# Performance work log

Hardware: AMD Instinct MI355X
Metric: run time of the kernel (lower is better)

Reference implementation:

```python
import jax, jax.numpy as jnp
import numpy as np
from jax import lax

B, N, F_IN, DIM = 128, 200, 200, 32
E_PER = 6400
K1, K2 = 100, 50
OUT = 2
BN_EPS = 1e-5


def setup_inputs():
    key = jax.random.key(0)
    ks = jax.random.split(key, 16)
    x = jax.random.normal(ks[0], (B * N, F_IN), jnp.float32)
    src = jax.random.randint(ks[1], (B, E_PER), 0, N)
    dst = jax.random.randint(ks[2], (B, E_PER), 0, N)
    off = (jnp.arange(B) * N)[:, None]
    edge_index = jnp.stack([(src + off).reshape(-1), (dst + off).reshape(-1)]).astype(jnp.int32)
    batch = jnp.repeat(jnp.arange(B, dtype=jnp.int32), N)

    def lin(k, i, o):
        kw, kb = jax.random.split(k)
        return (jax.random.normal(kw, (i, o), jnp.float32) / np.float32(np.sqrt(i)),
                jax.random.normal(kb, (o,), jnp.float32) * 0.01)

    w1a, b1a = lin(ks[3], F_IN, DIM)
    w1b, b1b = lin(ks[4], DIM, DIM)
    w2a, b2a = lin(ks[5], DIM, DIM)
    w2b, b2b = lin(ks[6], DIM, DIM)
    pw1 = jax.random.normal(ks[7], (DIM,), jnp.float32)
    pw2 = jax.random.normal(ks[8], (DIM,), jnp.float32)
    fc1_w, fc1_b = lin(ks[9], 2 * DIM, 4 * DIM)
    fc2_w, fc2_b = lin(ks[10], 4 * DIM, 8 * DIM)
    fc3_w, fc3_b = lin(ks[11], 8 * DIM, OUT)
    return dict(x=x, edge_index=edge_index, batch=batch,
                w1a=w1a, b1a=b1a, w1b=w1b, b1b=b1b,
                w2a=w2a, b2a=b2a, w2b=w2b, b2b=b2b,
                pw1=pw1, pw2=pw2,
                fc1_w=fc1_w, fc1_b=fc1_b, fc2_w=fc2_w, fc2_b=fc2_b,
                fc3_w=fc3_w, fc3_b=fc3_b,
                bn1_g=jnp.ones((4 * DIM,)), bn1_b=jnp.zeros((4 * DIM,)),
                bn1_m=jnp.zeros((4 * DIM,)), bn1_v=jnp.ones((4 * DIM,)),
                bn2_g=jnp.ones((8 * DIM,)), bn2_b=jnp.zeros((8 * DIM,)),
                bn2_m=jnp.zeros((8 * DIM,)), bn2_v=jnp.ones((8 * DIM,)))


def gin_conv(x, src, dst, valid, wa, ba, wb, bb, n_nodes):
    # PyG GINConv: mlp((1+eps)*x + sum_{j->i} x_j), eps=0 (default)
    msg = x[src]
    if valid is not None:
        msg = msg * valid[:, None]
    aggr = jax.ops.segment_sum(msg, dst, num_segments=n_nodes)
    h = jax.nn.relu((x + aggr) @ wa + ba)
    return h @ wb + bb


def topk_pool(x, src, dst, valid, pw, nb, n_per, k):
    # PyG TopKPooling: score = tanh((x.w)/||w||); keep top-k per graph; x <- x[perm]*score[perm]
    score = jnp.tanh((x @ pw) / jnp.linalg.norm(pw))
    topv, topi = lax.top_k(score.reshape(nb, n_per), k)  # [nb,k], descending (matches PyG ordering)
    perm = (topi + (jnp.arange(nb) * n_per)[:, None]).reshape(-1)
    x_new = x[perm] * topv.reshape(-1, 1)
    new_id = jnp.full((nb * n_per,), -1, jnp.int32).at[perm].set(jnp.arange(nb * k, dtype=jnp.int32))
    s, d = new_id[src], new_id[dst]
    v = (s >= 0) & (d >= 0)
    if valid is not None:
        v = v & valid
    return x_new, jnp.maximum(s, 0), jnp.maximum(d, 0), v, topv


def bn_eval(h, g, b, m, v):
    return (h - m) * lax.rsqrt(v + BN_EPS) * g + b


def reference(x, edge_index, batch,
              w1a, b1a, w1b, b1b, w2a, b2a, w2b, b2b, pw1, pw2,
              fc1_w, fc1_b, fc2_w, fc2_b, fc3_w, fc3_b,
              bn1_g, bn1_b, bn1_m, bn1_v, bn2_g, bn2_b, bn2_m, bn2_v):
    src, dst = edge_index[0], edge_index[1]
    h = jax.nn.relu(gin_conv(x, src, dst, None, w1a, b1a, w1b, b1b, B * N))
    h, src, dst, valid, attn1 = topk_pool(h, src, dst, None, pw1, B, N, K1)
    hb = h.reshape(B, K1, DIM)
    x1 = jnp.concatenate([hb.max(axis=1), hb.mean(axis=1)], axis=1)  # gmp || gap
    h = jax.nn.relu(gin_conv(h, src, dst, valid.astype(h.dtype), w2a, b2a, w2b, b2b, B * K1))
    h, src, dst, valid, attn2 = topk_pool(h, src, dst, valid, pw2, B, K1, K2)
    hb = h.reshape(B, K2, DIM)
    x2 = jnp.concatenate([hb.max(axis=1), hb.mean(axis=1)], axis=1)
    z = x1 + x2
    z = bn_eval(jax.nn.relu(z @ fc1_w + fc1_b), bn1_g, bn1_b, bn1_m, bn1_v)  # dropout p=0.6 inactive (eval)
    z = bn_eval(jax.nn.relu(z @ fc2_w + fc2_b), bn2_g, bn2_b, bn2_m, bn2_v)
    xy = jax.nn.log_softmax(z @ fc3_w + fc3_b, axis=-1)
    return xy, jax.nn.sigmoid(attn1), jax.nn.sigmoid(attn2)
```

## Files before the change

### kernel.cpp

```cpp
#include <hip/hip_runtime.h>
#include <math.h>

#define NGRAPH 128
#define NNODE  200
#define FIN    200
#define DIM    32
#define EPER   6400
#define ETOT   819200
#define KP1    100
#define KP2    50

#define W1B_OFF  0
#define W2A_OFF  1024
#define W2B_OFF  2048
#define B1A_OFF  3072
#define B1B_OFF  3104
#define B2A_OFF  3136
#define B2B_OFF  3168
#define PW1_OFF  3200
#define PW2_OFF  3232
#define NRM1_OFF 3264
#define NRM2_OFF 3265
#define SW_SIZE  3280

__device__ __forceinline__ int swz(int row, int chunk) {
  return (row << 5) + (((chunk ^ ((row >> 2) & 7))) << 2);
}

__device__ __forceinline__ void lds_spin(volatile int* f, int target) {
  while (*f != target) __builtin_amdgcn_s_sleep(2);
}

template <int ROWS, bool RELU, bool BIAS, bool FUSE, bool SCORE>
__device__ __forceinline__ void mm2r(const float* __restrict__ A,
                                     const float* __restrict__ A2,
                                     const float* __restrict__ fb,
                                     const float* __restrict__ W,
                                     float* __restrict__ O,
                                     const float* __restrict__ bias,
                                     const float* __restrict__ pw,
                                     const float* __restrict__ nrmp,
                                     float* __restrict__ scoreOut, int tid) {
  if (tid < ROWS * 2) {
    const int rg = tid >> 2, cg = tid & 3;
    const int r0 = rg * 2, d0 = cg * 8;
    float acc[2][8];
#pragma unroll
    for (int r = 0; r < 2; ++r)
#pragma unroll
      for (int c = 0; c < 8; ++c) acc[r][c] = 0.f;
#pragma unroll
    for (int kc = 0; kc < 8; ++kc) {
      float4 av[2];
#pragma unroll
      for (int r = 0; r < 2; ++r) {
        const int p = swz(r0 + r, kc);
        float4 v = *(const float4*)&A[p];
        if (FUSE) {
          const float4 u = *(const float4*)&A2[p];
          const float4 b = *(const float4*)&fb[kc * 4];
          v.x = fmaxf(v.x + u.x + b.x, 0.f);
          v.y = fmaxf(v.y + u.y + b.y, 0.f);
          v.z = fmaxf(v.z + u.z + b.z, 0.f);
          v.w = fmaxf(v.w + u.w + b.w, 0.f);
        }
        av[r] = v;
      }
#pragma unroll
      for (int j = 0; j < 4; ++j) {
        const int k = kc * 4 + j;
        const float4 wa = *(const float4*)&W[k * 32 + d0];
        const float4 wb = *(const float4*)&W[k * 32 + d0 + 4];
#pragma unroll
        for (int r = 0; r < 2; ++r) {
          const float xs = (j == 0) ? av[r].x : (j == 1) ? av[r].y
                                  : (j == 2) ? av[r].z : av[r].w;
          acc[r][0] += xs * wa.x; acc[r][1] += xs * wa.y;
          acc[r][2] += xs * wa.z; acc[r][3] += xs * wa.w;
          acc[r][4] += xs * wb.x; acc[r][5] += xs * wb.y;
          acc[r][6] += xs * wb.z; acc[r][7] += xs * wb.w;
        }
      }
    }
    float dot[2] = {0.f, 0.f};
#pragma unroll
    for (int r = 0; r < 2; ++r) {
      float v[8];
#pragma unroll
      for (int c = 0; c < 8; ++c) {
        float t = acc[r][c];
        if (BIAS) t += bias[d0 + c];
        if (RELU) t = fmaxf(t, 0.f);
        v[c] = t;
      }
      if (SCORE) {
        float d = 0.f;
#pragma unroll
        for (int c = 0; c < 8; ++c) d += v[c] * pw[d0 + c];
        dot[r] = d;
      }
      float4 o0, o1;
      o0.x = v[0]; o0.y = v[1]; o0.z = v[2]; o0.w = v[3];
      o1.x = v[4]; o1.y = v[5]; o1.z = v[6]; o1.w = v[7];
      *(float4*)&O[swz(r0 + r, cg * 2)] = o0;
      *(float4*)&O[swz(r0 + r, cg * 2 + 1)] = o1;
    }
    if (SCORE) {
      dot[0] += __shfl_xor(dot[0], 1); dot[0] += __shfl_xor(dot[0], 2);
      dot[1] += __shfl_xor(dot[1], 1); dot[1] += __shfl_xor(dot[1], 2);
      if ((tid & 3) == 0) {
        const float nrm = *nrmp;
        scoreOut[r0] = tanhf(dot[0] / nrm);
        scoreOut[r0 + 1] = tanhf(dot[1] / nrm);
      }
    }
  }
}

__device__ __forceinline__ void scan_counts(const int* __restrict__ cnt,
                                            int* __restrict__ start, int lane) {
  const int b = lane * 4;
  const int c0 = (cnt[b + 0] + 3) & ~3;
  const int c1 = (cnt[b + 1] + 3) & ~3;
  const int c2 = (cnt[b + 2] + 3) & ~3;
  const int c3 = (cnt[b + 3] + 3) & ~3;
  const int t01 = c0 + c1;
  const int t012 = t01 + c2;
  const int tot = t012 + c3;
  int run = tot;
#pragma unroll
  for (int off = 1; off < 64; off <<= 1) {
    const int t = __shfl_up(run, off);
    if (lane >= off) run += t;
  }
  const int e = run - tot;
  start[b + 0] = e;
  start[b + 1] = e + c0;
  start[b + 2] = e + t01;
  start[b + 3] = e + t012;
}

template <int NN>
__device__ __forceinline__ void aggregate(const float* __restrict__ sYv,
                                          float* __restrict__ sAgv,
                                          const int* __restrict__ sSrcv,
                                          const int* __restrict__ sStartv,
                                          const int* __restrict__ sCntv, int tid) {
  const int slot = tid >> 3, part = tid & 7;
#pragma unroll
  for (int p = 0; p < (NN + 127) / 128; ++p) {
    const int n = p * 128 + slot;
    if (n < NN) {
      const int jb = sStartv[n];
      const int je = jb + sCntv[n];
      float4 a0 = {0, 0, 0, 0}, a1 = {0, 0, 0, 0}, a2 = {0, 0, 0, 0}, a3 = {0, 0, 0, 0};
      int j = jb;
      for (; j + 4 <= je; j += 4) {
        const int4 ss = *(const int4*)&sSrcv[j];
        const float4 v0 = *(const float4*)&sYv[swz(ss.x, part)];
        const float4 v1 = *(const float4*)&sYv[swz(ss.y, part)];
        const float4 v2 = *(const float4*)&sYv[swz(ss.z, part)];
        const float4 v3 = *(const float4*)&sYv[swz(ss.w, part)];
        a0.x += v0.x; a0.y += v0.y; a0.z += v0.z; a0.w += v0.w;
        a1.x += v1.x; a1.y += v1.y; a1.z += v1.z; a1.w += v1.w;
        a2.x += v2.x; a2.y += v2.y; a2.z += v2.z; a2.w += v2.w;
        a3.x += v3.x; a3.y += v3.y; a3.z += v3.z; a3.w += v3.w;
      }
      for (; j < je; ++j) {
        const float4 v = *(const float4*)&sYv[swz(sSrcv[j], part)];
        a0.x += v.x; a0.y += v.y; a0.z += v.z; a0.w += v.w;
      }
      float4 o;
      o.x = (a0.x + a1.x) + (a2.x + a3.x);
      o.y = (a0.y + a1.y) + (a2.y + a3.y);
      o.z = (a0.z + a1.z) + (a2.z + a3.z);
      o.w = (a0.w + a1.w) + (a2.w + a3.w);
      *(float4*)&sAgv[swz(n, part)] = o;
    }
  }
}

__global__ __launch_bounds__(1024, 1) void gin_fused(
    const float* __restrict__ x, const int* __restrict__ ei,
    const float* __restrict__ w1a, const float* __restrict__ b1a,
    const float* __restrict__ w1b, const float* __restrict__ b1b,
    const float* __restrict__ w2a, const float* __restrict__ b2a,
    const float* __restrict__ w2b, const float* __restrict__ b2b,
    const float* __restrict__ pw1, const float* __restrict__ pw2,
    const float* __restrict__ fc1w, const float* __restrict__ fc1b,
    const float* __restrict__ fc2w, const float* __restrict__ fc2b,
    const float* __restrict__ fc3w, const float* __restrict__ fc3b,
    const float* __restrict__ bn1g, const float* __restrict__ bn1b,
    const float* __restrict__ bn1m, const float* __restrict__ bn1v,
    const float* __restrict__ bn2g, const float* __restrict__ bn2b,
    const float* __restrict__ bn2m, const float* __restrict__ bn2v,
    float* __restrict__ out) {
  __shared__ __align__(16) float sY[6400];
  __shared__ __align__(16) float sAg[6400];
  __shared__ __align__(16) float sH[6400];
  __shared__ __align__(16) float sHp[3200];
  __shared__ __align__(16) float sW[SW_SIZE];
  __shared__ __align__(16) int sSrc[7040];
  __shared__ unsigned short sEdge[6400];
  __shared__ int sCnt[256], sStart[256], sOfs[256];
  __shared__ int sCnt2[256], sStart2[256], sOfs2[256];
  __shared__ int sFlag[4];
  __shared__ float sScore[256];
  __shared__ int sNewid[256];
  __shared__ float sZ[64];
  __shared__ float sZ1[128];
  __shared__ float sZ2[256];
  __shared__ float sLg[2];

  const int tid = threadIdx.x;
  const int g = blockIdx.x;

  if (tid < 256) {
    for (int i = tid; i < 1600; i += 256)
      *(float4*)&sAg[i * 4] = ((const float4*)w1a)[i];
    if (tid < 32) {
      sW[B1A_OFF + tid] = b1a[tid];
      sW[B1B_OFF + tid] = b1b[tid];
      sW[B2A_OFF + tid] = b2a[tid];
      sW[B2B_OFF + tid] = b2b[tid];
      sW[PW1_OFF + tid] = pw1[tid];
      sW[PW2_OFF + tid] = pw2[tid];
    }
  } else if (tid < 512) {
    const int t = tid - 256;
    for (int i = t; i < 768; i += 256) {
      const float4 v = (i < 256) ? ((const float4*)w1b)[i]
                    : (i < 512) ? ((const float4*)w2a)[i - 256]
                                : ((const float4*)w2b)[i - 512];
      const int off = (i < 256) ? W1B_OFF + i * 4
                    : (i < 512) ? W2A_OFF + (i - 256) * 4
                                : W2B_OFF + (i - 512) * 4;
      *(float4*)&sW[off] = v;
    }
    for (int i = t; i < 256; i += 256) {
      sCnt[i] = 0; sOfs[i] = 0; sCnt2[i] = 0; sOfs2[i] = 0;
    }
    if (t < 4) sFlag[t] = 0;
  } else {
    const int eb = g * EPER, nb = g * NNODE;
    for (int i = tid - 512; i < EPER / 4; i += 512) {
      const int4 ss = *(const int4*)&ei[eb + i * 4];
      const int4 dd = *(const int4*)&ei[ETOT + eb + i * 4];
      sEdge[i * 4 + 0] = (unsigned short)(((ss.x - nb) << 8) | (dd.x - nb));
      sEdge[i * 4 + 1] = (unsigned short)(((ss.y - nb) << 8) | (dd.y - nb));
      sEdge[i * 4 + 2] = (unsigned short)(((ss.z - nb) << 8) | (dd.z - nb));
      sEdge[i * 4 + 3] = (unsigned short)(((ss.w - nb) << 8) | (dd.w - nb));
    }
  }
  __syncthreads();

  if (tid < 200) {
    const int rg = tid >> 2, cg = tid & 3;
    const int n0 = rg * 4, d0 = cg * 8;
    float acc[4][8];
#pragma unroll
    for (int r = 0; r < 4; ++r)
#pragma unroll
      for (int c = 0; c < 8; ++c) acc[r][c] = 0.f;
    const float* xg = x + ((size_t)g * NNODE + n0) * FIN;
    for (int k = 0; k < FIN; k += 4) {
      float4 xv[4];
#pragma unroll
      for (int r = 0; r < 4; ++r)
        xv[r] = *(const float4*)&xg[r * FIN + k];
#pragma unroll
      for (int j = 0; j < 4; ++j) {
        const float4 wa = *(const float4*)&sAg[(k + j) * 32 + d0];
        const float4 wb = *(const float4*)&sAg[(k + j) * 32 + d0 + 4];
#pragma unroll
        for (int r = 0; r < 4; ++r) {
          const float xs = (j == 0) ? xv[r].x : (j == 1) ? xv[r].y
                                   : (j == 2) ? xv[r].z : xv[r].w;
          acc[r][0] += xs * wa.x; acc[r][1] += xs * wa.y;
          acc[r][2] += xs * wa.z; acc[r][3] += xs * wa.w;
          acc[r][4] += xs * wb.x; acc[r][5] += xs * wb.y;
          acc[r][6] += xs * wb.z; acc[r][7] += xs * wb.w;
        }
      }
    }
#pragma unroll
    for (int r = 0; r < 4; ++r) {
      float4 o0, o1;
      o0.x = acc[r][0]; o0.y = acc[r][1]; o0.z = acc[r][2]; o0.w = acc[r][3];
      o1.x = acc[r][4]; o1.y = acc[r][5]; o1.z = acc[r][6]; o1.w = acc[r][7];
      *(float4*)&sY[swz(n0 + r, cg * 2)] = o0;
      *(float4*)&sY[swz(n0 + r, cg * 2 + 1)] = o1;
    }
  } else if (tid == 200) {
    float s = 0.f;
    for (int k = 0; k < 32; ++k) s += sW[PW1_OFF + k] * sW[PW1_OFF + k];
    sW[NRM1_OFF] = sqrtf(s);
  } else if (tid == 201) {
    float s = 0.f;
    for (int k = 0; k < 32; ++k) s += sW[PW2_OFF + k] * sW[PW2_OFF + k];
    sW[NRM2_OFF] = sqrtf(s);
  } else if (tid >= 256) {
    const int t = tid - 256;
    for (int e = t; e < EPER; e += 768)
      atomicAdd(&sCnt[sEdge[e] & 255], 1);
    __threadfence_block();
    atomicAdd(&sFlag[0], 1);
    if (tid >= 960) {
      lds_spin(&sFlag[0], 768);
      __threadfence_block();
      scan_counts(sCnt, sStart, tid - 960);
      __threadfence_block();
      if (tid == 960) atomicExch(&sFlag[1], 1);
    }
    lds_spin(&sFlag[1], 1);
    __threadfence_block();
    for (int e = t; e < EPER; e += 768) {
      const unsigned short p = sEdge[e];
      sSrc[sStart[p & 255] + atomicAdd(&sOfs[p & 255], 1)] = p >> 8;
    }
  }
  __syncthreads();

  aggregate<NNODE>(sY, sAg, sSrc, sStart, sCnt, tid);
  __syncthreads();

  mm2r<200, true, true, true, true>(sY, sAg, &sW[B1A_OFF], &sW[W1B_OFF], sH,
                                    &sW[B1B_OFF], &sW[PW1_OFF], &sW[NRM1_OFF],
                                    sScore, tid);
  __syncthreads();

  if (tid < NNODE * 4) {
    const int n = tid >> 2, q = tid & 3;
    const float s = sScore[n];
    int r = 0;
    for (int m = q * 50; m < q * 50 + 50; ++m) {
      const float sm = sScore[m];
      r += (sm > s) || (sm == s && m < n);
    }
    r += __shfl_xor(r, 1);
    r += __shfl_xor(r, 2);
    if (q == 0) {
      sNewid[n] = (r < KP1) ? r : -1;
      if (r < KP1) out[2 * NGRAPH + g * KP1 + r] = 1.f / (1.f + expf(-s));
    }
    if (r < KP1) {
#pragma unroll
      for (int c = 0; c < 2; ++c) {
        const int ch = q * 2 + c;
        float4 v = *(const float4*)&sH[swz(n, ch)];
        v.x *= s; v.y *= s; v.z *= s; v.w *= s;
        *(float4*)&sHp[swz(r, ch)] = v;
      }
    }
  }
  __syncthreads();

  mm2r<KP1, false, false, false, false>(sHp, nullptr, nullptr, &sW[W2A_OFF],
                                        sY, nullptr, nullptr, nullptr, nullptr,
                                        tid);
  if (tid >= 256 && tid < 288) {
    const int t = tid - 256;
    const int ch = t >> 2, w = t & 3;
    float m0 = -INFINITY, m1 = -INFINITY, s0 = 0.f, s1 = 0.f;
    for (int r = 0; r < KP1; r += 2) {
      const float v0 = sHp[swz(r, ch) + w];
      const float v1 = sHp[swz(r + 1, ch) + w];
      m0 = fmaxf(m0, v0); m1 = fmaxf(m1, v1);
      s0 += v0; s1 += v1;
    }
    sZ[t] = fmaxf(m0, m1);
    sZ[32 + t] = (s0 + s1) / (float)KP1;
  } else if (tid >= 512) {
    const int t = tid - 512;
    for (int e = t; e < EPER; e += 512) {
      const unsigned short p = sEdge[e];
      const int s1 = sNewid[p >> 8], d1 = sNewid[p & 255];
      if (s1 >= 0 && d1 >= 0) atomicAdd(&sCnt2[d1], 1);
    }
    __threadfence_block();
    atomicAdd(&sFlag[2], 1);
    if (tid >= 960) {
      lds_spin(&sFlag[2], 512);
      __threadfence_block();
      scan_counts(sCnt2, sStart2, tid - 960);
      __threadfence_block();
      if (tid == 960) atomicExch(&sFlag[3], 1);
    }
    lds_spin(&sFlag[3], 1);
    __threadfence_block();
    for (int e = t; e < EPER; e += 512) {
      const unsigned short p = sEdge[e];
      const int s1 = sNewid[p >> 8], d1 = sNewid[p & 255];
      if (s1 >= 0 && d1 >= 0)
        sSrc[sStart2[d1] + atomicAdd(&sOfs2[d1], 1)] = s1;
    }
  }
  __syncthreads();

  aggregate<KP1>(sY, sAg, sSrc, sStart2, sCnt2, tid);
  __syncthreads();

  mm2r<KP1, true, true, true, true>(sY, sAg, &sW[B2A_OFF], &sW[W2B_OFF], sH,
                                    &sW[B2B_OFF], &sW[PW2_OFF], &sW[NRM2_OFF],
                                    sScore, tid);
  __syncthreads();

  if (tid < KP1 * 4) {
    const int n = tid >> 2, q = tid & 3;
    const float s = sScore[n];
    int r = 0;
    for (int m = q * 25; m < q * 25 + 25; ++m) {
      const float sm = sScore[m];
      r += (sm > s) || (sm == s && m < n);
    }
    r += __shfl_xor(r, 1);
    r += __shfl_xor(r, 2);
    if (q == 0) {
      sNewid[n] = (r < KP2) ? r : -1;
      if (r < KP2)
        out[2 * NGRAPH + NGRAPH * KP1 + g * KP2 + r] = 1.f / (1.f + expf(-s));
    }
    if (r < KP2) {
#pragma unroll
      for (int c = 0; c < 2; ++c) {
        const int ch = q * 2 + c;
        float4 v = *(const float4*)&sH[swz(n, ch)];
        v.x *= s; v.y *= s; v.z *= s; v.w *= s;
        *(float4*)&sHp[swz(r, ch)] = v;
      }
    }
  }
  __syncthreads();

  if (tid < 32) {
    const int ch = tid >> 2, w = tid & 3;
    float m0 = -INFINITY, m1 = -INFINITY, s0 = 0.f, s1 = 0.f;
    for (int r = 0; r < KP2; r += 2) {
      const float v0 = sHp[swz(r, ch) + w];
      const float v1 = sHp[swz(r + 1, ch) + w];
      m0 = fmaxf(m0, v0); m1 = fmaxf(m1, v1);
      s0 += v0; s1 += v1;
    }
    sZ[tid] += fmaxf(m0, m1);
    sZ[32 + tid] += (s0 + s1) / (float)KP2;
  }
  __syncthreads();

  if (tid < 512) {
    const int o = tid >> 2, q = tid & 3;
    float a = 0.f;
    for (int k = q * 16; k < q * 16 + 16; ++k) a += sZ[k] * fc1w[k * 128 + o];
    a += __shfl_xor(a, 1);
    a += __shfl_xor(a, 2);
    if (q == 0) {
      a += fc1b[o];
      a = fmaxf(a, 0.f);
      a = (a - bn1m[o]) * rsqrtf(bn1v[o] + 1e-5f) * bn1g[o] + bn1b[o];
      sZ1[o] = a;
    }
  }
  __syncthreads();

  if (tid < 512) {
    const int o = tid >> 1, h = tid & 1;
    float a = 0.f;
    for (int k = h * 64; k < h * 64 + 64; ++k) a += sZ1[k] * fc2w[k * 256 + o];
    a += __shfl_xor(a, 1);
    if (h == 0) {
      a += fc2b[o];
      a = fmaxf(a, 0.f);
      a = (a - bn2m[o]) * rsqrtf(bn2v[o] + 1e-5f) * bn2g[o] + bn2b[o];
      sZ2[o] = a;
    }
  }
  __syncthreads();

  if (tid < 64) {
    const int k4 = tid * 4;
    float a0 = 0.f, a1 = 0.f;
#pragma unroll
    for (int k = 0; k < 4; ++k) {
      const float z = sZ2[k4 + k];
      a0 += z * fc3w[(k4 + k) * 2 + 0];
      a1 += z * fc3w[(k4 + k) * 2 + 1];
    }
#pragma unroll
    for (int off = 32; off; off >>= 1) {
      a0 += __shfl_xor(a0, off);
      a1 += __shfl_xor(a1, off);
    }
    if (tid == 0) {
      const float l0 = a0 + fc3b[0], l1 = a1 + fc3b[1];
      const float m = fmaxf(l0, l1);
      const float lse = m + logf(expf(l0 - m) + expf(l1 - m));
      out[g * 2 + 0] = l0 - lse;
      out[g * 2 + 1] = l1 - lse;
    }
  }
}

extern "C" void kernel_launch(void* const* d_in, const int* in_sizes, int n_in,
                              void* d_out, int out_size, void* d_ws,
                              size_t ws_size, hipStream_t stream) {
  (void)in_sizes; (void)n_in; (void)out_size; (void)d_ws; (void)ws_size;
  gin_fused<<<NGRAPH, 1024, 0, stream>>>(
      (const float*)d_in[0], (const int*)d_in[1],
      (const float*)d_in[3], (const float*)d_in[4],
      (const float*)d_in[5], (const float*)d_in[6],
      (const float*)d_in[7], (const float*)d_in[8],
      (const float*)d_in[9], (const float*)d_in[10],
      (const float*)d_in[11], (const float*)d_in[12],
      (const float*)d_in[13], (const float*)d_in[14],
      (const float*)d_in[15], (const float*)d_in[16],
      (const float*)d_in[17], (const float*)d_in[18],
      (const float*)d_in[19], (const float*)d_in[20],
      (const float*)d_in[21], (const float*)d_in[22],
      (const float*)d_in[23], (const float*)d_in[24],
      (const float*)d_in[25], (const float*)d_in[26],
      (float*)d_out);
}
```

Before: 52.75 us.

## Split first-layer projection into producer blocks with global flag handoff

Launches twice as many blocks. The first 128 blocks compute the x@w1a projection for each graph using all 800 threads and write it to workspace, then release a per-graph flag. The consumer blocks build the CSR in parallel, spin on the flag, and load the projection from global memory. The LDS spin-flag coordination is replaced with plain barriers, and the pooling reductions are split across two segments. This spreads the large input GEMM across more CUs, at the cost of an extra memset, a global round trip, and a deadlock risk if consumer blocks get scheduled before their producers.

```diff
diff --git a/kernel.cpp b/kernel.cpp
--- a/kernel.cpp
+++ b/kernel.cpp
@@ -25,10 +25,6 @@
 
 __device__ __forceinline__ int swz(int row, int chunk) {
   return (row << 5) + (((chunk ^ ((row >> 2) & 7))) << 2);
-}
-
-__device__ __forceinline__ void lds_spin(volatile int* f, int target) {
-  while (*f != target) __builtin_amdgcn_s_sleep(2);
 }
 
 template <int ROWS, bool RELU, bool BIAS, bool FUSE, bool SCORE>
@@ -194,6 +190,7 @@
     const float* __restrict__ bn1m, const float* __restrict__ bn1v,
     const float* __restrict__ bn2g, const float* __restrict__ bn2b,
     const float* __restrict__ bn2m, const float* __restrict__ bn2v,
+    int* __restrict__ flags, float* __restrict__ y1ws,
     float* __restrict__ out) {
   __shared__ __align__(16) float sY[6400];
   __shared__ __align__(16) float sAg[6400];
@@ -204,28 +201,60 @@
   __shared__ unsigned short sEdge[6400];
   __shared__ int sCnt[256], sStart[256], sOfs[256];
   __shared__ int sCnt2[256], sStart2[256], sOfs2[256];
-  __shared__ int sFlag[4];
   __shared__ float sScore[256];
   __shared__ int sNewid[256];
   __shared__ float sZ[64];
   __shared__ float sZ1[128];
   __shared__ float sZ2[256];
-  __shared__ float sLg[2];
 
   const int tid = threadIdx.x;
-  const int g = blockIdx.x;
+  const int bid = blockIdx.x;
+
+  if (bid < NGRAPH) {
+    const int g = bid;
+    for (int i = tid; i < 1600; i += 1024)
+      ((float4*)sAg)[i] = ((const float4*)w1a)[i];
+    __syncthreads();
+    if (tid < 800) {
+      const int rg = tid >> 3, cg = tid & 7;
+      const int n0 = rg * 2, d0 = cg * 4;
+      float a0[4] = {0, 0, 0, 0}, a1[4] = {0, 0, 0, 0};
+      const float* xg = x + ((size_t)g * NNODE + n0) * FIN;
+      for (int k = 0; k < FIN; k += 4) {
+        const float4 xa = *(const float4*)&xg[k];
+        const float4 xb = *(const float4*)&xg[FIN + k];
+#pragma unroll
+        for (int j = 0; j < 4; ++j) {
+          const float4 w = *(const float4*)&sAg[(k + j) * 32 + d0];
+          const float s0 = (j == 0) ? xa.x : (j == 1) ? xa.y
+                         : (j == 2) ? xa.z : xa.w;
+          const float s1 = (j == 0) ? xb.x : (j == 1) ? xb.y
+                         : (j == 2) ? xb.z : xb.w;
+          a0[0] += s0 * w.x; a0[1] += s0 * w.y;
+          a0[2] += s0 * w.z; a0[3] += s0 * w.w;
+          a1[0] += s1 * w.x; a1[1] += s1 * w.y;
+          a1[2] += s1 * w.z; a1[3] += s1 * w.w;
+        }
+      }
+      float* yg = y1ws + (size_t)g * 6400;
+      float4 o;
+      o.x = a0[0]; o.y = a0[1]; o.z = a0[2]; o.w = a0[3];
+      *(float4*)&yg[swz(n0, cg)] = o;
+      o.x = a1[0]; o.y = a1[1]; o.z = a1[2]; o.w = a1[3];
+      *(float4*)&yg[swz(n0 + 1, cg)] = o;
+    }
+    __threadfence();
+    __syncthreads();
+    if (tid == 0)
+      __hip_atomic_store(&flags[g], 1, __ATOMIC_RELEASE,
+                         __HIP_MEMORY_SCOPE_AGENT);
+    return;
+  }
+
+  const int g = bid - NGRAPH;
 
   if (tid < 256) {
-    for (int i = tid; i < 1600; i += 256)
-      *(float4*)&sAg[i * 4] = ((const float4*)w1a)[i];
-    if (tid < 32) {
-      sW[B1A_OFF + tid] = b1a[tid];
-      sW[B1B_OFF + tid] = b1b[tid];
-      sW[B2A_OFF + tid] = b2a[tid];
-      sW[B2B_OFF + tid] = b2b[tid];
-      sW[PW1_OFF + tid] = pw1[tid];
-      sW[PW2_OFF + tid] = pw2[tid];
-    }
+    sCnt[tid] = 0; sOfs[tid] = 0; sCnt2[tid] = 0; sOfs2[tid] = 0;
   } else if (tid < 512) {
     const int t = tid - 256;
     for (int i = t; i < 768; i += 256) {
@@ -237,10 +266,14 @@
                                 : W2B_OFF + (i - 512) * 4;
       *(float4*)&sW[off] = v;
     }
-    for (int i = t; i < 256; i += 256) {
-      sCnt[i] = 0; sOfs[i] = 0; sCnt2[i] = 0; sOfs2[i] = 0;
-    }
-    if (t < 4) sFlag[t] = 0;
+    if (t < 32) {
+      sW[B1A_OFF + t] = b1a[t];
+      sW[B1B_OFF + t] = b1b[t];
+      sW[B2A_OFF + t] = b2a[t];
+      sW[B2B_OFF + t] = b2b[t];
+      sW[PW1_OFF + t] = pw1[t];
+      sW[PW2_OFF + t] = pw2[t];
+    }
   } else {
     const int eb = g * EPER, nb = g * NNODE;
     for (int i = tid - 512; i < EPER / 4; i += 512) {
@@ -254,70 +287,45 @@
   }
   __syncthreads();
 
-  if (tid < 200) {
-    const int rg = tid >> 2, cg = tid & 3;
-    const int n0 = rg * 4, d0 = cg * 8;
-    float acc[4][8];
-#pragma unroll
-    for (int r = 0; r < 4; ++r)
-#pragma unroll
-      for (int c = 0; c < 8; ++c) acc[r][c] = 0.f;
-    const float* xg = x + ((size_t)g * NNODE + n0) * FIN;
-    for (int k = 0; k < FIN; k += 4) {
-      float4 xv[4];
-#pragma unroll
-      for (int r = 0; r < 4; ++r)
-        xv[r] = *(const float4*)&xg[r * FIN + k];
-#pragma unroll
-      for (int j = 0; j < 4; ++j) {
-        const float4 wa = *(const float4*)&sAg[(k + j) * 32 + d0];
-        const float4 wb = *(const float4*)&sAg[(k + j) * 32 + d0 + 4];
-#pragma unroll
-        for (int r = 0; r < 4; ++r) {
-          const float xs = (j == 0) ? xv[r].x : (j == 1) ? xv[r].y
-                                   : (j == 2) ? xv[r].z : xv[r].w;
-          acc[r][0] += xs * wa.x; acc[r][1] += xs * wa.y;
-          acc[r][2] += xs * wa.z; acc[r][3] += xs * wa.w;
-          acc[r][4] += xs * wb.x; acc[r][5] += xs * wb.y;
-          acc[r][6] += xs * wb.z; acc[r][7] += xs * wb.w;
-        }
-      }
-    }
-#pragma unroll
-    for (int r = 0; r < 4; ++r) {
-      float4 o0, o1;
-      o0.x = acc[r][0]; o0.y = acc[r][1]; o0.z = acc[r][2]; o0.w = acc[r][3];
-      o1.x = acc[r][4]; o1.y = acc[r][5]; o1.z = acc[r][6]; o1.w = acc[r][7];
-      *(float4*)&sY[swz(n0 + r, cg * 2)] = o0;
-      *(float4*)&sY[swz(n0 + r, cg * 2 + 1)] = o1;
-    }
-  } else if (tid == 200) {
+  if (tid < 800) {
+    const uint4 u = *(const uint4*)&sEdge[tid * 8];
+    atomicAdd(&sCnt[u.x & 255], 1);
+    atomicAdd(&sCnt[(u.x >> 16) & 255], 1);
+    atomicAdd(&sCnt[u.y & 255], 1);
+    atomicAdd(&sCnt[(u.y >> 16) & 255], 1);
+    atomicAdd(&sCnt[u.z & 255], 1);
+    atomicAdd(&sCnt[(u.z >> 16) & 255], 1);
+    atomicAdd(&sCnt[u.w & 255], 1);
+    atomicAdd(&sCnt[(u.w >> 16) & 255], 1);
+  } else if (tid == 1022) {
     float s = 0.f;
     for (int k = 0; k < 32; ++k) s += sW[PW1_OFF + k] * sW[PW1_OFF + k];
     sW[NRM1_OFF] = sqrtf(s);
-  } else if (tid == 201) {
+  } else if (tid == 1023) {
     float s = 0.f;
     for (int k = 0; k < 32; ++k) s += sW[PW2_OFF + k] * sW[PW2_OFF + k];
     sW[NRM2_OFF] = sqrtf(s);
-  } else if (tid >= 256) {
-    const int t = tid - 256;
-    for (int e = t; e < EPER; e += 768)
-      atomicAdd(&sCnt[sEdge[e] & 255], 1);
-    __threadfence_block();
-    atomicAdd(&sFlag[0], 1);
-    if (tid >= 960) {
-      lds_spin(&sFlag[0], 768);
-      __threadfence_block();
-      scan_counts(sCnt, sStart, tid - 960);
-      __threadfence_block();
-      if (tid == 960) atomicExch(&sFlag[1], 1);
-    }
-    lds_spin(&sFlag[1], 1);
-    __threadfence_block();
-    for (int e = t; e < EPER; e += 768) {
+  }
+  __syncthreads();
+
+  if (tid < 64) scan_counts(sCnt, sStart, tid);
+  __syncthreads();
+
+  if (tid < 1020) {
+    for (int e = tid; e < EPER; e += 1020) {
       const unsigned short p = sEdge[e];
       sSrc[sStart[p & 255] + atomicAdd(&sOfs[p & 255], 1)] = p >> 8;
     }
+  } else if (tid == 1023) {
+    while (__hip_atomic_load(&flags[g], __ATOMIC_ACQUIRE,
+                             __HIP_MEMORY_SCOPE_AGENT) == 0)
+      __builtin_amdgcn_s_sleep(8);
+  }
+  __syncthreads();
+
+  {
+    const float4* src = (const float4*)(y1ws + (size_t)g * 6400);
+    for (int i = tid; i < 1600; i += 1024) ((float4*)sY)[i] = src[i];
   }
   __syncthreads();
 
@@ -358,42 +366,38 @@
   mm2r<KP1, false, false, false, false>(sHp, nullptr, nullptr, &sW[W2A_OFF],
                                         sY, nullptr, nullptr, nullptr, nullptr,
                                         tid);
-  if (tid >= 256 && tid < 288) {
-    const int t = tid - 256;
-    const int ch = t >> 2, w = t & 3;
-    float m0 = -INFINITY, m1 = -INFINITY, s0 = 0.f, s1 = 0.f;
-    for (int r = 0; r < KP1; r += 2) {
-      const float v0 = sHp[swz(r, ch) + w];
-      const float v1 = sHp[swz(r + 1, ch) + w];
-      m0 = fmaxf(m0, v0); m1 = fmaxf(m1, v1);
-      s0 += v0; s1 += v1;
-    }
-    sZ[t] = fmaxf(m0, m1);
-    sZ[32 + t] = (s0 + s1) / (float)KP1;
+  if (tid >= 256 && tid < 320) {
+    const int l = tid - 256;
+    const int idx = l & 31, seg = l >> 5;
+    const int ch = idx >> 2, w = idx & 3;
+    float m = -INFINITY, s = 0.f;
+    for (int r = seg * 50; r < seg * 50 + 50; ++r) {
+      const float v = sHp[swz(r, ch) + w];
+      m = fmaxf(m, v); s += v;
+    }
+    m = fmaxf(m, __shfl_xor(m, 32));
+    s += __shfl_xor(s, 32);
+    if (seg == 0) {
+      sZ[idx] = m;
+      sZ[32 + idx] = s / (float)KP1;
+    }
   } else if (tid >= 512) {
-    const int t = tid - 512;
-    for (int e = t; e < EPER; e += 512) {
+    for (int e = tid - 512; e < EPER; e += 512) {
       const unsigned short p = sEdge[e];
       const int s1 = sNewid[p >> 8], d1 = sNewid[p & 255];
       if (s1 >= 0 && d1 >= 0) atomicAdd(&sCnt2[d1], 1);
     }
-    __threadfence_block();
-    atomicAdd(&sFlag[2], 1);
-    if (tid >= 960) {
-      lds_spin(&sFlag[2], 512);
-      __threadfence_block();
-      scan_counts(sCnt2, sStart2, tid - 960);
-      __threadfence_block();
-      if (tid == 960) atomicExch(&sFlag[3], 1);
-    }
-    lds_spin(&sFlag[3], 1);
-    __threadfence_block();
-    for (int e = t; e < EPER; e += 512) {
-      const unsigned short p = sEdge[e];
-      const int s1 = sNewid[p >> 8], d1 = sNewid[p & 255];
-      if (s1 >= 0 && d1 >= 0)
-        sSrc[sStart2[d1] + atomicAdd(&sOfs2[d1], 1)] = s1;
-    }
+  }
+  __syncthreads();
+
+  if (tid < 64) scan_counts(sCnt2, sStart2, tid);
+  __syncthreads();
+
+  for (int e = tid; e < EPER; e += 1024) {
+    const unsigned short p = sEdge[e];
+    const int s1 = sNewid[p >> 8], d1 = sNewid[p & 255];
+    if (s1 >= 0 && d1 >= 0)
+      sSrc[sStart2[d1] + atomicAdd(&sOfs2[d1], 1)] = s1;
   }
   __syncthreads();
 
@@ -432,17 +436,20 @@
   }
   __syncthreads();
 
-  if (tid < 32) {
-    const int ch = tid >> 2, w = tid & 3;
-    float m0 = -INFINITY, m1 = -INFINITY, s0 = 0.f, s1 = 0.f;
-    for (int r = 0; r < KP2; r += 2) {
-      const float v0 = sHp[swz(r, ch) + w];
-      const float v1 = sHp[swz(r + 1, ch) + w];
-      m0 = fmaxf(m0, v0); m1 = fmaxf(m1, v1);
-      s0 += v0; s1 += v1;
-    }
-    sZ[tid] += fmaxf(m0, m1);
-    sZ[32 + tid] += (s0 + s1) / (float)KP2;
+  if (tid < 64) {
+    const int idx = tid & 31, seg = tid >> 5;
+    const int ch = idx >> 2, w = idx & 3;
+    float m = -INFINITY, s = 0.f;
+    for (int r = seg * 25; r < seg * 25 + 25; ++r) {
+      const float v = sHp[swz(r, ch) + w];
+      m = fmaxf(m, v); s += v;
+    }
+    m = fmaxf(m, __shfl_xor(m, 32));
+    s += __shfl_xor(s, 32);
+    if (seg == 0) {
+      sZ[idx] += m;
+      sZ[32 + idx] += s / (float)KP2;
+    }
   }
   __syncthreads();
 
@@ -502,8 +509,11 @@
 extern "C" void kernel_launch(void* const* d_in, const int* in_sizes, int n_in,
                               void* d_out, int out_size, void* d_ws,
                               size_t ws_size, hipStream_t stream) {
-  (void)in_sizes; (void)n_in; (void)out_size; (void)d_ws; (void)ws_size;
-  gin_fused<<<NGRAPH, 1024, 0, stream>>>(
+  (void)in_sizes; (void)n_in; (void)out_size; (void)ws_size;
+  int* flags = (int*)d_ws;
+  float* y1ws = (float*)((char*)d_ws + 4096);
+  hipMemsetAsync(d_ws, 0, 4096, stream);
+  gin_fused<<<2 * NGRAPH, 1024, 0, stream>>>(
       (const float*)d_in[0], (const int*)d_in[1],
       (const float*)d_in[3], (const float*)d_in[4],
       (const float*)d_in[5], (const float*)d_in[6],
@@ -517,5 +527,5 @@
       (const float*)d_in[21], (const float*)d_in[22],
       (const float*)d_in[23], (const float*)d_in[24],
       (const float*)d_in[25], (const float*)d_in[26],
-      (float*)d_out);
+      flags, y1ws, (float*)d_out);
 }
```

Result: slower. 139.5 us (+164.4%).

## Replace block barriers with wave-level flags and fuse MLP head into one wave

Applied to the files above, without the earlier changes.

The first layer's prologue now uses per-wave LDS flag counters instead of a full __syncthreads. The w1a load gates the node GEMM directly, and the edge-load, histogram, scan and CSR-fill stages run on the other waves concurrently, with the remaining weight loads deferred to after the CSR fill. The GEMM K-loop is unrolled by 8, and pooling reductions are split across two half-waves with a shuffle combine. The fc1/fc2/fc3 head is collapsed into a single 64-thread wave so three block barriers disappear. This removes barrier stalls and tail latency but serialises the head MLP onto fewer threads with longer loops.

```diff
diff --git a/kernel.cpp b/kernel.cpp
--- a/kernel.cpp
+++ b/kernel.cpp
@@ -27,8 +27,10 @@
   return (row << 5) + (((chunk ^ ((row >> 2) & 7))) << 2);
 }
 
-__device__ __forceinline__ void lds_spin(volatile int* f, int target) {
-  while (*f != target) __builtin_amdgcn_s_sleep(2);
+__device__ __forceinline__ void spin_eq(const int* f, int target) {
+  while (__hip_atomic_load(f, __ATOMIC_RELAXED,
+                           __HIP_MEMORY_SCOPE_WORKGROUP) != target)
+    __builtin_amdgcn_s_sleep(1);
 }
 
 template <int ROWS, bool RELU, bool BIAS, bool FUSE, bool SCORE>
@@ -204,119 +206,140 @@
   __shared__ unsigned short sEdge[6400];
   __shared__ int sCnt[256], sStart[256], sOfs[256];
   __shared__ int sCnt2[256], sStart2[256], sOfs2[256];
-  __shared__ int sFlag[4];
+  __shared__ int sFlag[8];
   __shared__ float sScore[256];
   __shared__ int sNewid[256];
   __shared__ float sZ[64];
   __shared__ float sZ1[128];
-  __shared__ float sZ2[256];
-  __shared__ float sLg[2];
 
   const int tid = threadIdx.x;
+  const int lane = tid & 63;
   const int g = blockIdx.x;
+
+  if (tid < 8) sFlag[tid] = 0;
+  __syncthreads();
 
   if (tid < 256) {
     for (int i = tid; i < 1600; i += 256)
-      *(float4*)&sAg[i * 4] = ((const float4*)w1a)[i];
-    if (tid < 32) {
-      sW[B1A_OFF + tid] = b1a[tid];
-      sW[B1B_OFF + tid] = b1b[tid];
-      sW[B2A_OFF + tid] = b2a[tid];
-      sW[B2B_OFF + tid] = b2b[tid];
-      sW[PW1_OFF + tid] = pw1[tid];
-      sW[PW2_OFF + tid] = pw2[tid];
-    }
-  } else if (tid < 512) {
+      ((float4*)sAg)[i] = ((const float4*)w1a)[i];
+    __threadfence_block();
+    if (lane == 0) atomicAdd(&sFlag[0], 1);
+    spin_eq(&sFlag[0], 4);
+    if (tid < 200) {
+      const int rg = tid >> 2, cg = tid & 3;
+      const int n0 = rg * 4, d0 = cg * 8;
+      float acc[4][8];
+#pragma unroll
+      for (int r = 0; r < 4; ++r)
+#pragma unroll
+        for (int c = 0; c < 8; ++c) acc[r][c] = 0.f;
+      const float* xg = x + ((size_t)g * NNODE + n0) * FIN;
+      for (int k = 0; k < FIN; k += 8) {
+        float4 xv[4][2];
+#pragma unroll
+        for (int r = 0; r < 4; ++r) {
+          xv[r][0] = *(const float4*)&xg[r * FIN + k];
+          xv[r][1] = *(const float4*)&xg[r * FIN + k + 4];
+        }
+#pragma unroll
+        for (int h = 0; h < 2; ++h) {
+#pragma unroll
+          for (int j = 0; j < 4; ++j) {
+            const int kk = k + h * 4 + j;
+            const float4 wa = *(const float4*)&sAg[kk * 32 + d0];
+            const float4 wb = *(const float4*)&sAg[kk * 32 + d0 + 4];
+#pragma unroll
+            for (int r = 0; r < 4; ++r) {
+              const float xs = (j == 0) ? xv[r][h].x : (j == 1) ? xv[r][h].y
+                             : (j == 2) ? xv[r][h].z : xv[r][h].w;
+              acc[r][0] += xs * wa.x; acc[r][1] += xs * wa.y;
+              acc[r][2] += xs * wa.z; acc[r][3] += xs * wa.w;
+              acc[r][4] += xs * wb.x; acc[r][5] += xs * wb.y;
+              acc[r][6] += xs * wb.z; acc[r][7] += xs * wb.w;
+            }
+          }
+        }
+      }
+#pragma unroll
+      for (int r = 0; r < 4; ++r) {
+        float4 o0, o1;
+        o0.x = acc[r][0]; o0.y = acc[r][1]; o0.z = acc[r][2]; o0.w = acc[r][3];
+        o1.x = acc[r][4]; o1.y = acc[r][5]; o1.z = acc[r][6]; o1.w = acc[r][7];
+        *(float4*)&sY[swz(n0 + r, cg * 2)] = o0;
+        *(float4*)&sY[swz(n0 + r, cg * 2 + 1)] = o1;
+      }
+    } else {
+      const int t = tid - 200;
+      if (t < 32) {
+        sW[B1A_OFF + t] = b1a[t];
+        sW[B1B_OFF + t] = b1b[t];
+        sW[B2A_OFF + t] = b2a[t];
+        sW[B2B_OFF + t] = b2b[t];
+        sW[PW1_OFF + t] = pw1[t];
+        sW[PW2_OFF + t] = pw2[t];
+      }
+      __threadfence_block();
+      if (tid == 232) {
+        float s = 0.f;
+        for (int k = 0; k < 32; ++k) s += sW[PW1_OFF + k] * sW[PW1_OFF + k];
+        sW[NRM1_OFF] = sqrtf(s);
+      } else if (tid == 233) {
+        float s = 0.f;
+        for (int k = 0; k < 32; ++k) s += sW[PW2_OFF + k] * sW[PW2_OFF + k];
+        sW[NRM2_OFF] = sqrtf(s);
+      }
+    }
+  } else {
     const int t = tid - 256;
-    for (int i = t; i < 768; i += 256) {
-      const float4 v = (i < 256) ? ((const float4*)w1b)[i]
-                    : (i < 512) ? ((const float4*)w2a)[i - 256]
-                                : ((const float4*)w2b)[i - 512];
-      const int off = (i < 256) ? W1B_OFF + i * 4
-                    : (i < 512) ? W2A_OFF + (i - 256) * 4
-                                : W2B_OFF + (i - 512) * 4;
-      *(float4*)&sW[off] = v;
-    }
-    for (int i = t; i < 256; i += 256) {
-      sCnt[i] = 0; sOfs[i] = 0; sCnt2[i] = 0; sOfs2[i] = 0;
-    }
-    if (t < 4) sFlag[t] = 0;
-  } else {
-    const int eb = g * EPER, nb = g * NNODE;
-    for (int i = tid - 512; i < EPER / 4; i += 512) {
-      const int4 ss = *(const int4*)&ei[eb + i * 4];
-      const int4 dd = *(const int4*)&ei[ETOT + eb + i * 4];
-      sEdge[i * 4 + 0] = (unsigned short)(((ss.x - nb) << 8) | (dd.x - nb));
-      sEdge[i * 4 + 1] = (unsigned short)(((ss.y - nb) << 8) | (dd.y - nb));
-      sEdge[i * 4 + 2] = (unsigned short)(((ss.z - nb) << 8) | (dd.z - nb));
-      sEdge[i * 4 + 3] = (unsigned short)(((ss.w - nb) << 8) | (dd.w - nb));
-    }
-  }
-  __syncthreads();
-
-  if (tid < 200) {
-    const int rg = tid >> 2, cg = tid & 3;
-    const int n0 = rg * 4, d0 = cg * 8;
-    float acc[4][8];
-#pragma unroll
-    for (int r = 0; r < 4; ++r)
-#pragma unroll
-      for (int c = 0; c < 8; ++c) acc[r][c] = 0.f;
-    const float* xg = x + ((size_t)g * NNODE + n0) * FIN;
-    for (int k = 0; k < FIN; k += 4) {
-      float4 xv[4];
-#pragma unroll
-      for (int r = 0; r < 4; ++r)
-        xv[r] = *(const float4*)&xg[r * FIN + k];
-#pragma unroll
-      for (int j = 0; j < 4; ++j) {
-        const float4 wa = *(const float4*)&sAg[(k + j) * 32 + d0];
-        const float4 wb = *(const float4*)&sAg[(k + j) * 32 + d0 + 4];
-#pragma unroll
-        for (int r = 0; r < 4; ++r) {
-          const float xs = (j == 0) ? xv[r].x : (j == 1) ? xv[r].y
-                                   : (j == 2) ? xv[r].z : xv[r].w;
-          acc[r][0] += xs * wa.x; acc[r][1] += xs * wa.y;
-          acc[r][2] += xs * wa.z; acc[r][3] += xs * wa.w;
-          acc[r][4] += xs * wb.x; acc[r][5] += xs * wb.y;
-          acc[r][6] += xs * wb.z; acc[r][7] += xs * wb.w;
-        }
-      }
-    }
-#pragma unroll
-    for (int r = 0; r < 4; ++r) {
-      float4 o0, o1;
-      o0.x = acc[r][0]; o0.y = acc[r][1]; o0.z = acc[r][2]; o0.w = acc[r][3];
-      o1.x = acc[r][4]; o1.y = acc[r][5]; o1.z = acc[r][6]; o1.w = acc[r][7];
-      *(float4*)&sY[swz(n0 + r, cg * 2)] = o0;
-      *(float4*)&sY[swz(n0 + r, cg * 2 + 1)] = o1;
-    }
-  } else if (tid == 200) {
-    float s = 0.f;
-    for (int k = 0; k < 32; ++k) s += sW[PW1_OFF + k] * sW[PW1_OFF + k];
-    sW[NRM1_OFF] = sqrtf(s);
-  } else if (tid == 201) {
-    float s = 0.f;
-    for (int k = 0; k < 32; ++k) s += sW[PW2_OFF + k] * sW[PW2_OFF + k];
-    sW[NRM2_OFF] = sqrtf(s);
-  } else if (tid >= 256) {
-    const int t = tid - 256;
-    for (int e = t; e < EPER; e += 768)
-      atomicAdd(&sCnt[sEdge[e] & 255], 1);
+    if (t < 256) { sCnt[t] = 0; sOfs[t] = 0; sCnt2[t] = 0; sOfs2[t] = 0; }
+    {
+      const int eb = g * EPER, nb = g * NNODE;
+      for (int i = t; i < EPER / 4; i += 768) {
+        const int4 ss = *(const int4*)&ei[eb + i * 4];
+        const int4 dd = *(const int4*)&ei[ETOT + eb + i * 4];
+        sEdge[i * 4 + 0] = (unsigned short)(((ss.x - nb) << 8) | (dd.x - nb));
+        sEdge[i * 4 + 1] = (unsigned short)(((ss.y - nb) << 8) | (dd.y - nb));
+        sEdge[i * 4 + 2] = (unsigned short)(((ss.z - nb) << 8) | (dd.z - nb));
+        sEdge[i * 4 + 3] = (unsigned short)(((ss.w - nb) << 8) | (dd.w - nb));
+      }
+    }
     __threadfence_block();
-    atomicAdd(&sFlag[0], 1);
+    if (lane == 0) atomicAdd(&sFlag[1], 1);
+    spin_eq(&sFlag[1], 12);
+    for (int i = t; i < 800; i += 768) {
+      const uint4 u = *(const uint4*)&sEdge[i * 8];
+      atomicAdd(&sCnt[u.x & 255], 1);
+      atomicAdd(&sCnt[(u.x >> 16) & 255], 1);
+      atomicAdd(&sCnt[u.y & 255], 1);
+      atomicAdd(&sCnt[(u.y >> 16) & 255], 1);
+      atomicAdd(&sCnt[u.z & 255], 1);
+      atomicAdd(&sCnt[(u.z >> 16) & 255], 1);
+      atomicAdd(&sCnt[u.w & 255], 1);
+      atomicAdd(&sCnt[(u.w >> 16) & 255], 1);
+    }
+    __threadfence_block();
+    if (lane == 0) atomicAdd(&sFlag[2], 1);
     if (tid >= 960) {
-      lds_spin(&sFlag[0], 768);
-      __threadfence_block();
+      spin_eq(&sFlag[2], 12);
       scan_counts(sCnt, sStart, tid - 960);
       __threadfence_block();
-      if (tid == 960) atomicExch(&sFlag[1], 1);
-    }
-    lds_spin(&sFlag[1], 1);
-    __threadfence_block();
+      if (tid == 960) atomicExch(&sFlag[3], 1);
+    }
+    spin_eq(&sFlag[3], 1);
     for (int e = t; e < EPER; e += 768) {
       const unsigned short p = sEdge[e];
       sSrc[sStart[p & 255] + atomicAdd(&sOfs[p & 255], 1)] = p >> 8;
+    }
+    if (tid >= 512) {
+      for (int i = tid - 512; i < 768; i += 512) {
+        const float4 v = (i < 256) ? ((const float4*)w1b)[i]
+                      : (i < 512) ? ((const float4*)w2a)[i - 256]
+                                  : ((const float4*)w2b)[i - 512];
+        const int off = (i < 256) ? W1B_OFF + i * 4
+                      : (i < 512) ? W2A_OFF + (i - 256) * 4
+                                  : W2B_OFF + (i - 512) * 4;
+        *(float4*)&sW[off] = v;
+      }
     }
   }
   __syncthreads();
@@ -358,37 +381,37 @@
   mm2r<KP1, false, false, false, false>(sHp, nullptr, nullptr, &sW[W2A_OFF],
                                         sY, nullptr, nullptr, nullptr, nullptr,
                                         tid);
-  if (tid >= 256 && tid < 288) {
-    const int t = tid - 256;
-    const int ch = t >> 2, w = t & 3;
-    float m0 = -INFINITY, m1 = -INFINITY, s0 = 0.f, s1 = 0.f;
-    for (int r = 0; r < KP1; r += 2) {
-      const float v0 = sHp[swz(r, ch) + w];
-      const float v1 = sHp[swz(r + 1, ch) + w];
-      m0 = fmaxf(m0, v0); m1 = fmaxf(m1, v1);
-      s0 += v0; s1 += v1;
-    }
-    sZ[t] = fmaxf(m0, m1);
-    sZ[32 + t] = (s0 + s1) / (float)KP1;
+  if (tid >= 256 && tid < 320) {
+    const int l = tid - 256;
+    const int idx = l & 31, seg = l >> 5;
+    const int ch = idx >> 2, w = idx & 3;
+    float m = -INFINITY, s = 0.f;
+    for (int r = seg * 50; r < seg * 50 + 50; ++r) {
+      const float v = sHp[swz(r, ch) + w];
+      m = fmaxf(m, v); s += v;
+    }
+    m = fmaxf(m, __shfl_xor(m, 32));
+    s += __shfl_xor(s, 32);
+    if (seg == 0) {
+      sZ[idx] = m;
+      sZ[32 + idx] = s / (float)KP1;
+    }
   } else if (tid >= 512) {
-    const int t = tid - 512;
-    for (int e = t; e < EPER; e += 512) {
+    for (int e = tid - 512; e < EPER; e += 512) {
       const unsigned short p = sEdge[e];
       const int s1 = sNewid[p >> 8], d1 = sNewid[p & 255];
       if (s1 >= 0 && d1 >= 0) atomicAdd(&sCnt2[d1], 1);
     }
     __threadfence_block();
-    atomicAdd(&sFlag[2], 1);
+    if (lane == 0) atomicAdd(&sFlag[4], 1);
     if (tid >= 960) {
-      lds_spin(&sFlag[2], 512);
-      __threadfence_block();
+      spin_eq(&sFlag[4], 8);
       scan_counts(sCnt2, sStart2, tid - 960);
       __threadfence_block();
-      if (tid == 960) atomicExch(&sFlag[3], 1);
-    }
-    lds_spin(&sFlag[3], 1);
-    __threadfence_block();
-    for (int e = t; e < EPER; e += 512) {
+      if (tid == 960) atomicExch(&sFlag[5], 1);
+    }
+    spin_eq(&sFlag[5], 1);
+    for (int e = tid - 512; e < EPER; e += 512) {
       const unsigned short p = sEdge[e];
       const int s1 = sNewid[p >> 8], d1 = sNewid[p & 255];
       if (s1 >= 0 && d1 >= 0)
@@ -432,67 +455,67 @@
   }
   __syncthreads();
 
-  if (tid < 32) {
-    const int ch = tid >> 2, w = tid & 3;
-    float m0 = -INFINITY, m1 = -INFINITY, s0 = 0.f, s1 = 0.f;
-    for (int r = 0; r < KP2; r += 2) {
-      const float v0 = sHp[swz(r, ch) + w];
-      const float v1 = sHp[swz(r + 1, ch) + w];
-      m0 = fmaxf(m0, v0); m1 = fmaxf(m1, v1);
-      s0 += v0; s1 += v1;
-    }
-    sZ[tid] += fmaxf(m0, m1);
-    sZ[32 + tid] += (s0 + s1) / (float)KP2;
-  }
-  __syncthreads();
-
-  if (tid < 512) {
-    const int o = tid >> 2, q = tid & 3;
-    float a = 0.f;
-    for (int k = q * 16; k < q * 16 + 16; ++k) a += sZ[k] * fc1w[k * 128 + o];
-    a += __shfl_xor(a, 1);
-    a += __shfl_xor(a, 2);
-    if (q == 0) {
-      a += fc1b[o];
-      a = fmaxf(a, 0.f);
-      a = (a - bn1m[o]) * rsqrtf(bn1v[o] + 1e-5f) * bn1g[o] + bn1b[o];
-      sZ1[o] = a;
-    }
-  }
-  __syncthreads();
-
-  if (tid < 512) {
-    const int o = tid >> 1, h = tid & 1;
-    float a = 0.f;
-    for (int k = h * 64; k < h * 64 + 64; ++k) a += sZ1[k] * fc2w[k * 256 + o];
-    a += __shfl_xor(a, 1);
-    if (h == 0) {
-      a += fc2b[o];
-      a = fmaxf(a, 0.f);
-      a = (a - bn2m[o]) * rsqrtf(bn2v[o] + 1e-5f) * bn2g[o] + bn2b[o];
-      sZ2[o] = a;
-    }
-  }
-  __syncthreads();
-
   if (tid < 64) {
-    const int k4 = tid * 4;
-    float a0 = 0.f, a1 = 0.f;
-#pragma unroll
-    for (int k = 0; k < 4; ++k) {
-      const float z = sZ2[k4 + k];
-      a0 += z * fc3w[(k4 + k) * 2 + 0];
-      a1 += z * fc3w[(k4 + k) * 2 + 1];
-    }
+    const int c = tid & 31, seg = tid >> 5;
+    const int ch = c >> 2, w = c & 3;
+    float m = -INFINITY, s = 0.f;
+    for (int r = seg * 25; r < seg * 25 + 25; ++r) {
+      const float v = sHp[swz(r, ch) + w];
+      m = fmaxf(m, v); s += v;
+    }
+    m = fmaxf(m, __shfl_xor(m, 32));
+    s += __shfl_xor(s, 32);
+    if (seg == 0) {
+      sZ[c] += m;
+      sZ[32 + c] += s / (float)KP2;
+    }
+    __threadfence_block();
+
+    const int l = tid;
+    float a1 = fc1b[l], a2 = fc1b[l + 64];
+    for (int k = 0; k < 64; ++k) {
+      const float zk = sZ[k];
+      a1 += zk * fc1w[k * 128 + l];
+      a2 += zk * fc1w[k * 128 + l + 64];
+    }
+    a1 = fmaxf(a1, 0.f);
+    a1 = (a1 - bn1m[l]) * rsqrtf(bn1v[l] + 1e-5f) * bn1g[l] + bn1b[l];
+    a2 = fmaxf(a2, 0.f);
+    a2 = (a2 - bn1m[l + 64]) * rsqrtf(bn1v[l + 64] + 1e-5f) * bn1g[l + 64] +
+         bn1b[l + 64];
+    sZ1[l] = a1;
+    sZ1[l + 64] = a2;
+    __threadfence_block();
+
+    const int o4 = l * 4;
+    float b0 = fc2b[o4], b1 = fc2b[o4 + 1], b2 = fc2b[o4 + 2], b3 = fc2b[o4 + 3];
+    for (int k = 0; k < 128; ++k) {
+      const float zk = sZ1[k];
+      const float4 wv = *(const float4*)&fc2w[k * 256 + o4];
+      b0 += zk * wv.x; b1 += zk * wv.y; b2 += zk * wv.z; b3 += zk * wv.w;
+    }
+    const float4 bm = *(const float4*)&bn2m[o4];
+    const float4 bv = *(const float4*)&bn2v[o4];
+    const float4 bg = *(const float4*)&bn2g[o4];
+    const float4 bb = *(const float4*)&bn2b[o4];
+    b0 = (fmaxf(b0, 0.f) - bm.x) * rsqrtf(bv.x + 1e-5f) * bg.x + bb.x;
+    b1 = (fmaxf(b1, 0.f) - bm.y) * rsqrtf(bv.y + 1e-5f) * bg.y + bb.y;
+    b2 = (fmaxf(b2, 0.f) - bm.z) * rsqrtf(bv.z + 1e-5f) * bg.z + bb.z;
+    b3 = (fmaxf(b3, 0.f) - bm.w) * rsqrtf(bv.w + 1e-5f) * bg.w + bb.w;
+
+    float a0s = b0 * fc3w[(o4 + 0) * 2 + 0] + b1 * fc3w[(o4 + 1) * 2 + 0] +
+                b2 * fc3w[(o4 + 2) * 2 + 0] + b3 * fc3w[(o4 + 3) * 2 + 0];
+    float a1s = b0 * fc3w[(o4 + 0) * 2 + 1] + b1 * fc3w[(o4 + 1) * 2 + 1] +
+                b2 * fc3w[(o4 + 2) * 2 + 1] + b3 * fc3w[(o4 + 3) * 2 + 1];
 #pragma unroll
     for (int off = 32; off; off >>= 1) {
-      a0 += __shfl_xor(a0, off);
-      a1 += __shfl_xor(a1, off);
+      a0s += __shfl_xor(a0s, off);
+      a1s += __shfl_xor(a1s, off);
     }
     if (tid == 0) {
-      const float l0 = a0 + fc3b[0], l1 = a1 + fc3b[1];
-      const float m = fmaxf(l0, l1);
-      const float lse = m + logf(expf(l0 - m) + expf(l1 - m));
+      const float l0 = a0s + fc3b[0], l1 = a1s + fc3b[1];
+      const float mx = fmaxf(l0, l1);
+      const float lse = mx + logf(expf(l0 - mx) + expf(l1 - mx));
       out[g * 2 + 0] = l0 - lse;
       out[g * 2 + 1] = l1 - lse;
     }
```

After: 50.01 us. 5.2% less time.
